# Kernel optimization log

Measured on AMD Instinct MI355X. Metric: run time of the kernel, lower is better.

Reference implementation:

```python
import jax, jax.numpy as jnp
import numpy as np

EMBED = 1024
HEADS = 16
HEAD_DIM = EMBED // HEADS
EPS = 1e-8


def setup_inputs() -> dict:
    key = jax.random.key(0)
    ks = jax.random.split(key, 10)
    s = 1.0 / np.sqrt(EMBED)
    return {
        "hidden_input": jax.random.normal(ks[0], (4, 2048, EMBED), dtype=jnp.float32),
        "Wq": jax.random.uniform(ks[1], (EMBED, EMBED), jnp.float32, -s, s),
        "bq": jax.random.uniform(ks[2], (EMBED,), jnp.float32, -s, s),
        "Wk": jax.random.uniform(ks[3], (EMBED, EMBED), jnp.float32, -s, s),
        "bk": jax.random.uniform(ks[4], (EMBED,), jnp.float32, -s, s),
        "Wv": jax.random.uniform(ks[5], (EMBED, EMBED), jnp.float32, -s, s),
        "bv": jax.random.uniform(ks[6], (EMBED,), jnp.float32, -s, s),
        "Wp": jax.random.uniform(ks[7], (EMBED, EMBED), jnp.float32, -s, s),
        "bp": jax.random.uniform(ks[8], (EMBED,), jnp.float32, -s, s),
        "gamma": jnp.ones((EMBED,), jnp.float32),
        "beta": jnp.zeros((EMBED,), jnp.float32),
    }


def reference(hidden_input, Wq, bq, Wk, bk, Wv, bv, Wp, bp, gamma, beta):
    n, l, e = hidden_input.shape
    h, d = HEADS, HEAD_DIM

    def split_heads(x):  # [n, l, e] -> [n, h, l, d]
        return x.reshape(n, l, h, d).transpose(0, 2, 1, 3)

    q = split_heads(hidden_input @ Wq + bq)
    k = split_heads(hidden_input @ Wk + bk)
    v = split_heads(hidden_input @ Wv + bv)

    scores = jnp.einsum("nhqd,nhkd->nhqk", q, k) / jnp.sqrt(jnp.float32(d))
    attn = jax.nn.softmax(scores, axis=-1)
    ctx = jnp.einsum("nhqk,nhkd->nhqd", attn, v)
    ctx = ctx.transpose(0, 2, 1, 3).reshape(n, l, e)

    out = ctx @ Wp + bp
    x = out + hidden_input
    mu = jnp.mean(x, axis=-1, keepdims=True)
    var = jnp.mean(jnp.square(x - mu), axis=-1, keepdims=True)
    return (x - mu) / jnp.sqrt(var + EPS) * gamma + beta
```

## Files before the change

kernel.cpp:

```cpp
#include <hip/hip_runtime.h>

#define EMBED 1024
#define SEQ   2048
#define BATCH 4
#define HEADS 16

typedef __attribute__((ext_vector_type(8))) short short8;
typedef __attribute__((ext_vector_type(4))) float floatx4;

#define MFMA16(a, b, c) __builtin_amdgcn_mfma_f32_16x16x32_bf16((a), (b), (c), 0, 0, 0)
#define ATT_SCALE (0.125f * 1.44269504088896340736f)

static __device__ __forceinline__ unsigned short f2bf(float f) {
  union { float f; unsigned int u; } v; v.f = f;
  unsigned int u = v.u;
  u += 0x7fffu + ((u >> 16) & 1u);
  return (unsigned short)(u >> 16);
}

static __device__ __forceinline__ void async16(const unsigned short* g, unsigned short* l) {
  __builtin_amdgcn_global_load_lds(
      (const __attribute__((address_space(1))) void*)g,
      (__attribute__((address_space(3))) void*)l, 16, 0, 0);
}

__global__ __launch_bounds__(256) void k_cvt(const float* __restrict__ src,
                                             unsigned short* __restrict__ dst, int n8) {
  int i = blockIdx.x * 256 + threadIdx.x;
  if (i >= n8) return;
  const float4* s = (const float4*)src;
  float4 a = s[i * 2], b = s[i * 2 + 1];
  uint4 o;
  o.x = (unsigned)f2bf(a.x) | ((unsigned)f2bf(a.y) << 16);
  o.y = (unsigned)f2bf(a.z) | ((unsigned)f2bf(a.w) << 16);
  o.z = (unsigned)f2bf(b.x) | ((unsigned)f2bf(b.y) << 16);
  o.w = (unsigned)f2bf(b.z) | ((unsigned)f2bf(b.w) << 16);
  ((uint4*)dst)[i] = o;
}

__global__ __launch_bounds__(256) void k_wt(const float* __restrict__ Wq, const float* __restrict__ Wk,
                                            const float* __restrict__ Wv, const float* __restrict__ Wp,
                                            unsigned short* __restrict__ WT) {
  int z = blockIdx.z;
  const float* src = (z == 0) ? Wq : (z == 1) ? Wk : (z == 2) ? Wv : Wp;
  unsigned short* dst = WT + (size_t)z * EMBED * EMBED;
  int k0 = blockIdx.x * 64, n0 = blockIdx.y * 64;
  __shared__ unsigned short tile[64][65];
  int tid = threadIdx.x;
  for (int i = tid; i < 4096; i += 256) {
    int r = i >> 6, c = i & 63;
    tile[c][r] = f2bf(src[(size_t)(k0 + r) * EMBED + n0 + c]);
  }
  __syncthreads();
  for (int i = tid; i < 4096; i += 256) {
    int r = i >> 6, c = i & 63;
    dst[(size_t)(n0 + r) * EMBED + k0 + c] = tile[r][c];
  }
}

__global__ __launch_bounds__(256) void k_gemm_qkv(const unsigned short* __restrict__ A,
                                                  const unsigned short* __restrict__ BT,
                                                  const float* __restrict__ bq,
                                                  const float* __restrict__ bk,
                                                  const float* __restrict__ bv,
                                                  unsigned short* __restrict__ C) {
  __shared__ unsigned short Als[128 * 32];
  __shared__ unsigned short Bls[128 * 32];
  const int tid = threadIdx.x;
  const int m0 = blockIdx.y * 128, n0 = blockIdx.x * 128;
  const int w = tid >> 6, lane = tid & 63, l16 = lane & 15, quad = lane >> 4;
  const int wrow = (w >> 1) * 64, wcol = (w & 1) * 64;

  floatx4 acc[4][4];
#pragma unroll
  for (int i = 0; i < 4; ++i)
#pragma unroll
    for (int j = 0; j < 4; ++j) acc[i][j] = {0.f, 0.f, 0.f, 0.f};

  const int srow = tid >> 2;
  const int scol = (((tid & 3) ^ ((tid >> 3) & 3)) * 8);
  const unsigned short* Ap = A + (size_t)(m0 + srow) * EMBED + scol;
  const unsigned short* Bp = BT + (size_t)(n0 + srow) * EMBED + scol;

  for (int kt = 0; kt < 32; ++kt) {
    const int k0 = kt * 32;
    async16(Ap + k0, Als + tid * 8);
    async16(Ap + 64 * EMBED + k0, Als + 2048 + tid * 8);
    async16(Bp + k0, Bls + tid * 8);
    async16(Bp + 64 * EMBED + k0, Bls + 2048 + tid * 8);
    __syncthreads();
    short8 af[4], bf[4];
#pragma unroll
    for (int mt = 0; mt < 4; ++mt) {
      int row = wrow + mt * 16 + l16;
      af[mt] = *(const short8*)(Als + row * 32 + ((quad ^ ((row >> 1) & 3)) * 8));
    }
#pragma unroll
    for (int nt = 0; nt < 4; ++nt) {
      int row = wcol + nt * 16 + l16;
      bf[nt] = *(const short8*)(Bls + row * 32 + ((quad ^ ((row >> 1) & 3)) * 8));
    }
#pragma unroll
    for (int mt = 0; mt < 4; ++mt)
#pragma unroll
      for (int nt = 0; nt < 4; ++nt)
        acc[mt][nt] = MFMA16(af[mt], bf[nt], acc[mt][nt]);
    __syncthreads();
  }

  const float* bsel = (n0 < 1024) ? bq : (n0 < 2048 ? bk : bv);
  const int nb = n0 & 1023;
  float bias[4];
#pragma unroll
  for (int nt = 0; nt < 4; ++nt) bias[nt] = bsel[nb + wcol + nt * 16 + l16];
#pragma unroll
  for (int mt = 0; mt < 4; ++mt)
#pragma unroll
    for (int r = 0; r < 4; ++r) {
      int gm = m0 + wrow + mt * 16 + quad * 4 + r;
      size_t base = (size_t)gm * 3072 + n0 + wcol;
#pragma unroll
      for (int nt = 0; nt < 4; ++nt)
        C[base + nt * 16 + l16] = f2bf(acc[mt][nt][r] + bias[nt]);
    }
}

__global__ __launch_bounds__(256) void k_vt(const unsigned short* __restrict__ QKV,
                                            unsigned short* __restrict__ VT) {
  int lt = blockIdx.x;
  int bh = blockIdx.y;
  int b = bh >> 4, h = bh & 15;
  int l0 = lt * 64;
  __shared__ unsigned short tile[64][65];
  const unsigned short* src = QKV + (size_t)(b * SEQ) * 3072 + 2048 + h * 64;
  unsigned short* dst = VT + (size_t)bh * 64 * SEQ;
  int tid = threadIdx.x;
  for (int i = tid; i < 4096; i += 256) {
    int r = i >> 6, c = i & 63;
    tile[c][r] = src[(size_t)(l0 + r) * 3072 + c];
  }
  __syncthreads();
  for (int i = tid; i < 4096; i += 256) {
    int r = i >> 6, c = i & 63;
    dst[(size_t)r * SEQ + l0 + c] = tile[r][c];
  }
}

__global__ __launch_bounds__(256, 2) void k_attn(const unsigned short* __restrict__ QKV,
                                                 const unsigned short* __restrict__ VT,
                                                 unsigned short* __restrict__ CTX) {
  const int qt = blockIdx.x, bh = blockIdx.y;
  const int b = bh >> 4, h = bh & 15;
  const int tid = threadIdx.x;
  const int w = tid >> 6, lane = tid & 63, l16 = lane & 15, quad = lane >> 4;

  __shared__ unsigned short Kls[64 * 64];
  __shared__ unsigned short Vls[64 * 64];
  __shared__ unsigned short Pls[4][64 * 64];

  const unsigned short* Qb = QKV + (size_t)(b * SEQ + qt * 256 + w * 64) * 3072 + h * 64;
  const unsigned short* Kb = QKV + (size_t)(b * SEQ) * 3072 + 1024 + h * 64;
  const unsigned short* Vb = VT + (size_t)bh * 64 * SEQ;
  unsigned short* Pw = Pls[w];

  short8 qf[4][2];
#pragma unroll
  for (int mt = 0; mt < 4; ++mt)
#pragma unroll
    for (int kc = 0; kc < 2; ++kc)
      qf[mt][kc] = *(const short8*)(Qb + (size_t)(mt * 16 + l16) * 3072 + kc * 32 + quad * 8);

  floatx4 o[4][4];
  float rs[4][4];
#pragma unroll
  for (int mt = 0; mt < 4; ++mt)
#pragma unroll
    for (int nt = 0; nt < 4; ++nt) { o[mt][nt] = {0.f, 0.f, 0.f, 0.f}; rs[mt][nt] = 0.f; }

  const int srow = tid >> 3;
  const int scol = (((tid & 7) ^ (srow & 7)) * 8);

  for (int kt = 0; kt < 32; ++kt) {
    const int kv0 = kt * 64;
    async16(Kb + (size_t)(kv0 + srow) * 3072 + scol, Kls + tid * 8);
    async16(Kb + (size_t)(kv0 + 32 + srow) * 3072 + scol, Kls + 2048 + tid * 8);
    async16(Vb + (size_t)srow * SEQ + kv0 + scol, Vls + tid * 8);
    async16(Vb + (size_t)(32 + srow) * SEQ + kv0 + scol, Vls + 2048 + tid * 8);
    __syncthreads();

    short8 kf[4][2];
#pragma unroll
    for (int nt = 0; nt < 4; ++nt)
#pragma unroll
      for (int kc = 0; kc < 2; ++kc) {
        int row = nt * 16 + l16;
        kf[nt][kc] = *(const short8*)(Kls + row * 64 + (((kc * 4 + quad) ^ (row & 7)) * 8));
      }

#pragma unroll
    for (int mt = 0; mt < 4; ++mt) {
      floatx4 s[4];
#pragma unroll
      for (int nt = 0; nt < 4; ++nt) {
        floatx4 z = {0.f, 0.f, 0.f, 0.f};
        z = MFMA16(qf[mt][0], kf[nt][0], z);
        s[nt] = MFMA16(qf[mt][1], kf[nt][1], z);
      }
#pragma unroll
      for (int nt = 0; nt < 4; ++nt)
#pragma unroll
        for (int r = 0; r < 4; ++r) {
          float p = exp2f(s[nt][r] * ATT_SCALE);
          rs[mt][r] += p;
          int row = mt * 16 + quad * 4 + r;
          int col = nt * 16 + l16;
          union { float f; unsigned u; } cv; cv.f = p;
          Pw[row * 64 + (((col >> 3) ^ (row & 7)) * 8) + (col & 7)] = (unsigned short)(cv.u >> 16);
        }
    }

    __asm__ volatile("s_waitcnt lgkmcnt(0)" ::: "memory");

    short8 vf[4][2];
#pragma unroll
    for (int nt = 0; nt < 4; ++nt)
#pragma unroll
      for (int kc = 0; kc < 2; ++kc) {
        int row = nt * 16 + l16;
        vf[nt][kc] = *(const short8*)(Vls + row * 64 + (((kc * 4 + quad) ^ (row & 7)) * 8));
      }
#pragma unroll
    for (int kc = 0; kc < 2; ++kc)
#pragma unroll
      for (int mt = 0; mt < 4; ++mt) {
        int row = mt * 16 + l16;
        short8 pf = *(const short8*)(Pw + row * 64 + (((kc * 4 + quad) ^ (row & 7)) * 8));
#pragma unroll
        for (int nt = 0; nt < 4; ++nt)
          o[mt][nt] = MFMA16(pf, vf[nt][kc], o[mt][nt]);
      }
    __syncthreads();
  }

#pragma unroll
  for (int mt = 0; mt < 4; ++mt)
#pragma unroll
    for (int r = 0; r < 4; ++r) {
      float v = rs[mt][r];
#pragma unroll
      for (int off = 1; off < 16; off <<= 1) v += __shfl_xor(v, off);
      rs[mt][r] = 1.f / v;
    }

#pragma unroll
  for (int mt = 0; mt < 4; ++mt)
#pragma unroll
    for (int r = 0; r < 4; ++r) {
      int gq = b * SEQ + qt * 256 + w * 64 + mt * 16 + quad * 4 + r;
      float inv = rs[mt][r];
      size_t base = (size_t)gq * EMBED + h * 64;
#pragma unroll
      for (int nt = 0; nt < 4; ++nt)
        CTX[base + nt * 16 + l16] = f2bf(o[mt][nt][r] * inv);
    }
}

__global__ __launch_bounds__(256) void k_gemm_proj(const unsigned short* __restrict__ A,
                                                   const unsigned short* __restrict__ BT,
                                                   const float* __restrict__ bp,
                                                   const float* __restrict__ hid,
                                                   float* __restrict__ X) {
  __shared__ unsigned short Als[128 * 32];
  __shared__ unsigned short Bls[128 * 32];
  const int tid = threadIdx.x;
  const int m0 = blockIdx.y * 128, n0 = blockIdx.x * 128;
  const int w = tid >> 6, lane = tid & 63, l16 = lane & 15, quad = lane >> 4;
  const int wrow = (w >> 1) * 64, wcol = (w & 1) * 64;

  floatx4 acc[4][4];
#pragma unroll
  for (int i = 0; i < 4; ++i)
#pragma unroll
    for (int j = 0; j < 4; ++j) acc[i][j] = {0.f, 0.f, 0.f, 0.f};

  const int srow = tid >> 2;
  const int scol = (((tid & 3) ^ ((tid >> 3) & 3)) * 8);
  const unsigned short* Ap = A + (size_t)(m0 + srow) * EMBED + scol;
  const unsigned short* Bp = BT + (size_t)(n0 + srow) * EMBED + scol;

  for (int kt = 0; kt < 32; ++kt) {
    const int k0 = kt * 32;
    async16(Ap + k0, Als + tid * 8);
    async16(Ap + 64 * EMBED + k0, Als + 2048 + tid * 8);
    async16(Bp + k0, Bls + tid * 8);
    async16(Bp + 64 * EMBED + k0, Bls + 2048 + tid * 8);
    __syncthreads();
    short8 af[4], bf[4];
#pragma unroll
    for (int mt = 0; mt < 4; ++mt) {
      int row = wrow + mt * 16 + l16;
      af[mt] = *(const short8*)(Als + row * 32 + ((quad ^ ((row >> 1) & 3)) * 8));
    }
#pragma unroll
    for (int nt = 0; nt < 4; ++nt) {
      int row = wcol + nt * 16 + l16;
      bf[nt] = *(const short8*)(Bls + row * 32 + ((quad ^ ((row >> 1) & 3)) * 8));
    }
#pragma unroll
    for (int mt = 0; mt < 4; ++mt)
#pragma unroll
      for (int nt = 0; nt < 4; ++nt)
        acc[mt][nt] = MFMA16(af[mt], bf[nt], acc[mt][nt]);
    __syncthreads();
  }

  float bias[4];
#pragma unroll
  for (int nt = 0; nt < 4; ++nt) bias[nt] = bp[n0 + wcol + nt * 16 + l16];
#pragma unroll
  for (int mt = 0; mt < 4; ++mt)
#pragma unroll
    for (int r = 0; r < 4; ++r) {
      int gm = m0 + wrow + mt * 16 + quad * 4 + r;
      size_t base = (size_t)gm * EMBED + n0 + wcol;
#pragma unroll
      for (int nt = 0; nt < 4; ++nt) {
        size_t idx = base + nt * 16 + l16;
        X[idx] = acc[mt][nt][r] + bias[nt] + hid[idx];
      }
    }
}

__global__ __launch_bounds__(256) void k_ln(float* __restrict__ x,
                                            const float* __restrict__ gamma,
                                            const float* __restrict__ beta) {
  int row = blockIdx.x, tid = threadIdx.x;
  float4* rp = (float4*)(x + (size_t)row * EMBED);
  float4 v = rp[tid];
  float s = v.x + v.y + v.z + v.w;
  float q = v.x * v.x + v.y * v.y + v.z * v.z + v.w * v.w;
#pragma unroll
  for (int off = 1; off < 64; off <<= 1) {
    s += __shfl_xor(s, off);
    q += __shfl_xor(q, off);
  }
  __shared__ float ss[4], sq[4];
  int w = tid >> 6;
  if ((tid & 63) == 0) { ss[w] = s; sq[w] = q; }
  __syncthreads();
  s = ss[0] + ss[1] + ss[2] + ss[3];
  q = sq[0] + sq[1] + sq[2] + sq[3];
  float mean = s * (1.f / 1024.f);
  float var = q * (1.f / 1024.f) - mean * mean;
  float rstd = rsqrtf(var + 1e-8f);
  float4 g = ((const float4*)gamma)[tid];
  float4 be = ((const float4*)beta)[tid];
  v.x = (v.x - mean) * rstd * g.x + be.x;
  v.y = (v.y - mean) * rstd * g.y + be.y;
  v.z = (v.z - mean) * rstd * g.z + be.z;
  v.w = (v.w - mean) * rstd * g.w + be.w;
  rp[tid] = v;
}

extern "C" void kernel_launch(void* const* d_in, const int* in_sizes, int n_in,
                              void* d_out, int out_size, void* d_ws, size_t ws_size,
                              hipStream_t stream) {
  const float* hid   = (const float*)d_in[0];
  const float* Wq    = (const float*)d_in[1];
  const float* bq    = (const float*)d_in[2];
  const float* Wk    = (const float*)d_in[3];
  const float* bk    = (const float*)d_in[4];
  const float* Wv    = (const float*)d_in[5];
  const float* bv    = (const float*)d_in[6];
  const float* Wp    = (const float*)d_in[7];
  const float* bp    = (const float*)d_in[8];
  const float* gamma = (const float*)d_in[9];
  const float* beta  = (const float*)d_in[10];
  float* out = (float*)d_out;

  char* ws = (char*)d_ws;
  unsigned short* hidA = (unsigned short*)ws;
  unsigned short* WT   = (unsigned short*)(ws + (size_t)(16 << 20));
  unsigned short* QKV  = (unsigned short*)(ws + (size_t)(24 << 20));
  unsigned short* VT   = (unsigned short*)(ws + (size_t)(72 << 20));
  unsigned short* CTX  = (unsigned short*)(ws + (size_t)(88 << 20));

  k_cvt<<<4096, 256, 0, stream>>>(hid, hidA, (BATCH * SEQ * EMBED) / 8);
  k_wt<<<dim3(16, 16, 4), 256, 0, stream>>>(Wq, Wk, Wv, Wp, WT);
  k_gemm_qkv<<<dim3(24, 64), 256, 0, stream>>>(hidA, WT, bq, bk, bv, QKV);
  k_vt<<<dim3(32, 64), 256, 0, stream>>>(QKV, VT);
  k_attn<<<dim3(8, 64), 256, 0, stream>>>(QKV, VT, CTX);
  k_gemm_proj<<<dim3(8, 64), 256, 0, stream>>>(CTX, WT + (size_t)3 * EMBED * EMBED, bp, hid, out);
  k_ln<<<8192, 256, 0, stream>>>(out, gamma, beta);
}
```

Baseline: 340.7 us.

## Double-buffer K/V tiles in attention and split P into half-tiles

The attention kernel now double-buffers the K and V shared-memory tiles, prefetching tile kt+1 while tile kt is computed, which removes one barrier per iteration. The 64-column P tile is processed in two 32-column halves with a smaller padded and rotated P buffer. The smaller P buffer is meant to free LDS so that three blocks fit per CU. The grid axes are swapped so consecutive blocks cover different heads for the same query tile. The exchange is more complex indexing and higher register pressure under the tighter launch bound, and the single remaining barrier must still protect P reuse and buffer swaps correctly.

```diff
diff --git a/kernel.cpp b/kernel.cpp
--- a/kernel.cpp
+++ b/kernel.cpp
@@ -146,23 +146,32 @@
   }
 }
 
-__global__ __launch_bounds__(256, 2) void k_attn(const unsigned short* __restrict__ QKV,
+__global__ __launch_bounds__(256, 3) void k_attn(const unsigned short* __restrict__ QKV,
                                                  const unsigned short* __restrict__ VT,
                                                  unsigned short* __restrict__ CTX) {
-  const int qt = blockIdx.x, bh = blockIdx.y;
+  const int bh = blockIdx.x, qt = blockIdx.y;
   const int b = bh >> 4, h = bh & 15;
   const int tid = threadIdx.x;
   const int w = tid >> 6, lane = tid & 63, l16 = lane & 15, quad = lane >> 4;
-
-  __shared__ unsigned short Kls[64 * 64];
-  __shared__ unsigned short Vls[64 * 64];
-  __shared__ unsigned short Pls[4][64 * 64];
+  const int l7 = l16 & 7, h8 = l16 >> 3;
+
+  __shared__ unsigned short Kls[2][4096];
+  __shared__ unsigned short Vls[2][4096];
+  __shared__ unsigned short Pls[4][2560];
 
   const unsigned short* Qb = QKV + (size_t)(b * SEQ + qt * 256 + w * 64) * 3072 + h * 64;
   const unsigned short* Kb = QKV + (size_t)(b * SEQ) * 3072 + 1024 + h * 64;
   const unsigned short* Vb = VT + (size_t)bh * 64 * SEQ;
   unsigned short* Pw = Pls[w];
 
+  int pwb[4];
+#pragma unroll
+  for (int c0 = 0; c0 < 4; ++c0)
+    pwb[c0] = quad * 160 + (((h8 + quad + c0) & 3) << 3) + l7;
+  const int prb = l16 * 40 + (((quad + l16 + (l16 >> 2)) & 3) << 3);
+  const int sl0 = l16 * 64 + ((quad ^ l7) << 3);
+  const int sl1 = l16 * 64 + (((4 ^ quad) ^ l7) << 3);
+
   short8 qf[4][2];
 #pragma unroll
   for (int mt = 0; mt < 4; ++mt)
@@ -180,66 +189,65 @@
   const int srow = tid >> 3;
   const int scol = (((tid & 7) ^ (srow & 7)) * 8);
 
+  async16(Kb + (size_t)srow * 3072 + scol, Kls[0] + tid * 8);
+  async16(Kb + (size_t)(32 + srow) * 3072 + scol, Kls[0] + 2048 + tid * 8);
+  async16(Vb + (size_t)srow * SEQ + scol, Vls[0] + tid * 8);
+  async16(Vb + (size_t)(32 + srow) * SEQ + scol, Vls[0] + 2048 + tid * 8);
+
   for (int kt = 0; kt < 32; ++kt) {
-    const int kv0 = kt * 64;
-    async16(Kb + (size_t)(kv0 + srow) * 3072 + scol, Kls + tid * 8);
-    async16(Kb + (size_t)(kv0 + 32 + srow) * 3072 + scol, Kls + 2048 + tid * 8);
-    async16(Vb + (size_t)srow * SEQ + kv0 + scol, Vls + tid * 8);
-    async16(Vb + (size_t)(32 + srow) * SEQ + kv0 + scol, Vls + 2048 + tid * 8);
+    const int cur = kt & 1;
     __syncthreads();
-
-    short8 kf[4][2];
-#pragma unroll
-    for (int nt = 0; nt < 4; ++nt)
-#pragma unroll
-      for (int kc = 0; kc < 2; ++kc) {
-        int row = nt * 16 + l16;
-        kf[nt][kc] = *(const short8*)(Kls + row * 64 + (((kc * 4 + quad) ^ (row & 7)) * 8));
+    if (kt < 31) {
+      const int kv1 = (kt + 1) * 64;
+      async16(Kb + (size_t)(kv1 + srow) * 3072 + scol, Kls[cur ^ 1] + tid * 8);
+      async16(Kb + (size_t)(kv1 + 32 + srow) * 3072 + scol, Kls[cur ^ 1] + 2048 + tid * 8);
+      async16(Vb + (size_t)srow * SEQ + kv1 + scol, Vls[cur ^ 1] + tid * 8);
+      async16(Vb + (size_t)(32 + srow) * SEQ + kv1 + scol, Vls[cur ^ 1] + 2048 + tid * 8);
+    }
+    const unsigned short* K0 = Kls[cur];
+    const unsigned short* V0 = Vls[cur];
+
+#pragma unroll
+    for (int p = 0; p < 2; ++p) {
+      short8 kf[2][2];
+#pragma unroll
+      for (int ntp = 0; ntp < 2; ++ntp) {
+        kf[ntp][0] = *(const short8*)(K0 + sl0 + (2 * p + ntp) * 1024);
+        kf[ntp][1] = *(const short8*)(K0 + sl1 + (2 * p + ntp) * 1024);
       }
-
-#pragma unroll
-    for (int mt = 0; mt < 4; ++mt) {
-      floatx4 s[4];
-#pragma unroll
-      for (int nt = 0; nt < 4; ++nt) {
-        floatx4 z = {0.f, 0.f, 0.f, 0.f};
-        z = MFMA16(qf[mt][0], kf[nt][0], z);
-        s[nt] = MFMA16(qf[mt][1], kf[nt][1], z);
+#pragma unroll
+      for (int mt = 0; mt < 4; ++mt) {
+        floatx4 s0 = {0.f, 0.f, 0.f, 0.f}, s1 = {0.f, 0.f, 0.f, 0.f};
+        s0 = MFMA16(qf[mt][0], kf[0][0], s0);
+        s0 = MFMA16(qf[mt][1], kf[0][1], s0);
+        s1 = MFMA16(qf[mt][0], kf[1][0], s1);
+        s1 = MFMA16(qf[mt][1], kf[1][1], s1);
+#pragma unroll
+        for (int r = 0; r < 4; ++r) {
+          float p0 = exp2f(s0[r] * ATT_SCALE);
+          float p1 = exp2f(s1[r] * ATT_SCALE);
+          rs[mt][r] += p0 + p1;
+          union { float f; unsigned u; } c0v, c1v;
+          c0v.f = p0; c1v.f = p1;
+          Pw[pwb[r & 3] + (mt * 16 + r) * 40] = (unsigned short)(c0v.u >> 16);
+          Pw[pwb[(2 + r) & 3] + (mt * 16 + r) * 40] = (unsigned short)(c1v.u >> 16);
+        }
       }
+      __asm__ volatile("s_waitcnt lgkmcnt(0)" ::: "memory");
+
+      short8 vf[4];
 #pragma unroll
       for (int nt = 0; nt < 4; ++nt)
-#pragma unroll
-        for (int r = 0; r < 4; ++r) {
-          float p = exp2f(s[nt][r] * ATT_SCALE);
-          rs[mt][r] += p;
-          int row = mt * 16 + quad * 4 + r;
-          int col = nt * 16 + l16;
-          union { float f; unsigned u; } cv; cv.f = p;
-          Pw[row * 64 + (((col >> 3) ^ (row & 7)) * 8) + (col & 7)] = (unsigned short)(cv.u >> 16);
-        }
-    }
-
-    __asm__ volatile("s_waitcnt lgkmcnt(0)" ::: "memory");
-
-    short8 vf[4][2];
-#pragma unroll
-    for (int nt = 0; nt < 4; ++nt)
-#pragma unroll
-      for (int kc = 0; kc < 2; ++kc) {
-        int row = nt * 16 + l16;
-        vf[nt][kc] = *(const short8*)(Vls + row * 64 + (((kc * 4 + quad) ^ (row & 7)) * 8));
+        vf[nt] = *(const short8*)(V0 + (p ? sl1 : sl0) + nt * 1024);
+#pragma unroll
+      for (int mt = 0; mt < 4; ++mt) {
+        short8 pf = *(const short8*)(Pw + prb + mt * 640);
+#pragma unroll
+        for (int nt = 0; nt < 4; ++nt)
+          o[mt][nt] = MFMA16(pf, vf[nt], o[mt][nt]);
       }
-#pragma unroll
-    for (int kc = 0; kc < 2; ++kc)
-#pragma unroll
-      for (int mt = 0; mt < 4; ++mt) {
-        int row = mt * 16 + l16;
-        short8 pf = *(const short8*)(Pw + row * 64 + (((kc * 4 + quad) ^ (row & 7)) * 8));
-#pragma unroll
-        for (int nt = 0; nt < 4; ++nt)
-          o[mt][nt] = MFMA16(pf, vf[nt][kc], o[mt][nt]);
-      }
-    __syncthreads();
+      __asm__ volatile("" ::: "memory");
+    }
   }
 
 #pragma unroll
@@ -389,7 +397,7 @@
   k_wt<<<dim3(16, 16, 4), 256, 0, stream>>>(Wq, Wk, Wv, Wp, WT);
   k_gemm_qkv<<<dim3(24, 64), 256, 0, stream>>>(hidA, WT, bq, bk, bv, QKV);
   k_vt<<<dim3(32, 64), 256, 0, stream>>>(QKV, VT);
-  k_attn<<<dim3(8, 64), 256, 0, stream>>>(QKV, VT, CTX);
+  k_attn<<<dim3(64, 8), 256, 0, stream>>>(QKV, VT, CTX);
   k_gemm_proj<<<dim3(8, 64), 256, 0, stream>>>(CTX, WT + (size_t)3 * EMBED * EMBED, bp, hid, out);
   k_ln<<<8192, 256, 0, stream>>>(out, gamma, beta);
 }
```

After: 398.7 us. 1.17x slower.

## Double-buffer attention K/V loads, widen GEMM K-tile, and swap grid order

Applied to the files above, without the earlier changes.

The attention kernel now double-buffers K and V in shared memory. It prefetches the next tile right after the barrier, which removes the trailing barrier each iteration and overlaps global loads with compute. The P-tile write/read addressing switches to a rotated layout with precomputed offsets. Both GEMMs move from a K-tile of 32 to 64 with an 8-wide XOR swizzle, halving barrier count, and all three main kernels swap grid dimensions so consecutive blocks share the weight/K column tile. The cost is more LDS per block, which may lower occupancy, plus higher register pressure from loading V fragments early.

```diff
diff --git a/kernel.cpp b/kernel.cpp
--- a/kernel.cpp
+++ b/kernel.cpp
@@ -64,11 +64,12 @@
                                                   const float* __restrict__ bk,
                                                   const float* __restrict__ bv,
                                                   unsigned short* __restrict__ C) {
-  __shared__ unsigned short Als[128 * 32];
-  __shared__ unsigned short Bls[128 * 32];
+  __shared__ unsigned short Als[128 * 64];
+  __shared__ unsigned short Bls[128 * 64];
   const int tid = threadIdx.x;
-  const int m0 = blockIdx.y * 128, n0 = blockIdx.x * 128;
+  const int m0 = blockIdx.x * 128, n0 = blockIdx.y * 128;
   const int w = tid >> 6, lane = tid & 63, l16 = lane & 15, quad = lane >> 4;
+  const int l7 = l16 & 7;
   const int wrow = (w >> 1) * 64, wcol = (w & 1) * 64;
 
   floatx4 acc[4][4];
@@ -77,34 +78,45 @@
 #pragma unroll
     for (int j = 0; j < 4; ++j) acc[i][j] = {0.f, 0.f, 0.f, 0.f};
 
-  const int srow = tid >> 2;
-  const int scol = (((tid & 3) ^ ((tid >> 3) & 3)) * 8);
+  const int srow = tid >> 3;
+  const int scol = (((tid & 7) ^ (srow & 7)) * 8);
   const unsigned short* Ap = A + (size_t)(m0 + srow) * EMBED + scol;
   const unsigned short* Bp = BT + (size_t)(n0 + srow) * EMBED + scol;
 
-  for (int kt = 0; kt < 32; ++kt) {
-    const int k0 = kt * 32;
-    async16(Ap + k0, Als + tid * 8);
-    async16(Ap + 64 * EMBED + k0, Als + 2048 + tid * 8);
-    async16(Bp + k0, Bls + tid * 8);
-    async16(Bp + 64 * EMBED + k0, Bls + 2048 + tid * 8);
+  int ab[2], bb[2];
+#pragma unroll
+  for (int kc = 0; kc < 2; ++kc) {
+    ab[kc] = (wrow + l16) * 64 + (((4 * kc + quad) ^ l7) << 3);
+    bb[kc] = (wcol + l16) * 64 + (((4 * kc + quad) ^ l7) << 3);
+  }
+
+  for (int kt = 0; kt < 16; ++kt) {
+    const int k0 = kt * 64;
+#pragma unroll
+    for (int i = 0; i < 4; ++i)
+      async16(Ap + k0 + (size_t)i * 32 * EMBED, Als + i * 2048 + tid * 8);
+#pragma unroll
+    for (int i = 0; i < 4; ++i)
+      async16(Bp + k0 + (size_t)i * 32 * EMBED, Bls + i * 2048 + tid * 8);
     __syncthreads();
-    short8 af[4], bf[4];
-#pragma unroll
-    for (int mt = 0; mt < 4; ++mt) {
-      int row = wrow + mt * 16 + l16;
-      af[mt] = *(const short8*)(Als + row * 32 + ((quad ^ ((row >> 1) & 3)) * 8));
-    }
-#pragma unroll
-    for (int nt = 0; nt < 4; ++nt) {
-      int row = wcol + nt * 16 + l16;
-      bf[nt] = *(const short8*)(Bls + row * 32 + ((quad ^ ((row >> 1) & 3)) * 8));
-    }
+    short8 af[4][2], bf[4][2];
 #pragma unroll
     for (int mt = 0; mt < 4; ++mt)
 #pragma unroll
-      for (int nt = 0; nt < 4; ++nt)
-        acc[mt][nt] = MFMA16(af[mt], bf[nt], acc[mt][nt]);
+      for (int kc = 0; kc < 2; ++kc)
+        af[mt][kc] = *(const short8*)(Als + ab[kc] + mt * 1024);
+#pragma unroll
+    for (int nt = 0; nt < 4; ++nt)
+#pragma unroll
+      for (int kc = 0; kc < 2; ++kc)
+        bf[nt][kc] = *(const short8*)(Bls + bb[kc] + nt * 1024);
+#pragma unroll
+    for (int kc = 0; kc < 2; ++kc)
+#pragma unroll
+      for (int mt = 0; mt < 4; ++mt)
+#pragma unroll
+        for (int nt = 0; nt < 4; ++nt)
+          acc[mt][nt] = MFMA16(af[mt][kc], bf[nt][kc], acc[mt][nt]);
     __syncthreads();
   }
 
@@ -149,20 +161,32 @@
 __global__ __launch_bounds__(256, 2) void k_attn(const unsigned short* __restrict__ QKV,
                                                  const unsigned short* __restrict__ VT,
                                                  unsigned short* __restrict__ CTX) {
-  const int qt = blockIdx.x, bh = blockIdx.y;
+  const int bh = blockIdx.x, qt = blockIdx.y;
   const int b = bh >> 4, h = bh & 15;
   const int tid = threadIdx.x;
   const int w = tid >> 6, lane = tid & 63, l16 = lane & 15, quad = lane >> 4;
-
-  __shared__ unsigned short Kls[64 * 64];
-  __shared__ unsigned short Vls[64 * 64];
-  __shared__ unsigned short Pls[4][64 * 64];
+  const int l7 = l16 & 7, h8 = l16 >> 3;
+
+  __shared__ unsigned short Kls[2][4096];
+  __shared__ unsigned short Vls[2][4096];
+  __shared__ unsigned short Pls[4][4096];
 
   const unsigned short* Qb = QKV + (size_t)(b * SEQ + qt * 256 + w * 64) * 3072 + h * 64;
   const unsigned short* Kb = QKV + (size_t)(b * SEQ) * 3072 + 1024 + h * 64;
   const unsigned short* Vb = VT + (size_t)bh * 64 * SEQ;
   unsigned short* Pw = Pls[w];
 
+  int pwb[8];
+#pragma unroll
+  for (int s = 0; s < 8; ++s)
+    pwb[s] = quad * 256 + (((h8 + 4 * quad + s) & 7) << 3) + l7;
+  int prb[2], kvb[2];
+#pragma unroll
+  for (int kc = 0; kc < 2; ++kc) {
+    prb[kc] = l16 * 64 + (((4 * kc + quad + l16) & 7) << 3);
+    kvb[kc] = l16 * 64 + (((4 * kc + quad) ^ l7) << 3);
+  }
+
   short8 qf[4][2];
 #pragma unroll
   for (int mt = 0; mt < 4; ++mt)
@@ -180,21 +204,31 @@
   const int srow = tid >> 3;
   const int scol = (((tid & 7) ^ (srow & 7)) * 8);
 
+  async16(Kb + (size_t)srow * 3072 + scol, Kls[0] + tid * 8);
+  async16(Kb + (size_t)(32 + srow) * 3072 + scol, Kls[0] + 2048 + tid * 8);
+  async16(Vb + (size_t)srow * SEQ + scol, Vls[0] + tid * 8);
+  async16(Vb + (size_t)(32 + srow) * SEQ + scol, Vls[0] + 2048 + tid * 8);
+
   for (int kt = 0; kt < 32; ++kt) {
-    const int kv0 = kt * 64;
-    async16(Kb + (size_t)(kv0 + srow) * 3072 + scol, Kls + tid * 8);
-    async16(Kb + (size_t)(kv0 + 32 + srow) * 3072 + scol, Kls + 2048 + tid * 8);
-    async16(Vb + (size_t)srow * SEQ + kv0 + scol, Vls + tid * 8);
-    async16(Vb + (size_t)(32 + srow) * SEQ + kv0 + scol, Vls + 2048 + tid * 8);
+    const int cur = kt & 1;
     __syncthreads();
-
-    short8 kf[4][2];
+    if (kt < 31) {
+      const int kv1 = (kt + 1) * 64;
+      async16(Kb + (size_t)(kv1 + srow) * 3072 + scol, Kls[cur ^ 1] + tid * 8);
+      async16(Kb + (size_t)(kv1 + 32 + srow) * 3072 + scol, Kls[cur ^ 1] + 2048 + tid * 8);
+      async16(Vb + (size_t)srow * SEQ + kv1 + scol, Vls[cur ^ 1] + tid * 8);
+      async16(Vb + (size_t)(32 + srow) * SEQ + kv1 + scol, Vls[cur ^ 1] + 2048 + tid * 8);
+    }
+    const unsigned short* K0 = Kls[cur];
+    const unsigned short* V0 = Vls[cur];
+
+    short8 kf[4][2], vf[4][2];
 #pragma unroll
     for (int nt = 0; nt < 4; ++nt)
 #pragma unroll
       for (int kc = 0; kc < 2; ++kc) {
-        int row = nt * 16 + l16;
-        kf[nt][kc] = *(const short8*)(Kls + row * 64 + (((kc * 4 + quad) ^ (row & 7)) * 8));
+        kf[nt][kc] = *(const short8*)(K0 + kvb[kc] + nt * 1024);
+        vf[nt][kc] = *(const short8*)(V0 + kvb[kc] + nt * 1024);
       }
 
 #pragma unroll
@@ -212,34 +246,21 @@
         for (int r = 0; r < 4; ++r) {
           float p = exp2f(s[nt][r] * ATT_SCALE);
           rs[mt][r] += p;
-          int row = mt * 16 + quad * 4 + r;
-          int col = nt * 16 + l16;
           union { float f; unsigned u; } cv; cv.f = p;
-          Pw[row * 64 + (((col >> 3) ^ (row & 7)) * 8) + (col & 7)] = (unsigned short)(cv.u >> 16);
+          Pw[pwb[(r + 2 * nt) & 7] + mt * 1024 + r * 64] = (unsigned short)(cv.u >> 16);
         }
     }
-
     __asm__ volatile("s_waitcnt lgkmcnt(0)" ::: "memory");
 
-    short8 vf[4][2];
-#pragma unroll
-    for (int nt = 0; nt < 4; ++nt)
-#pragma unroll
-      for (int kc = 0; kc < 2; ++kc) {
-        int row = nt * 16 + l16;
-        vf[nt][kc] = *(const short8*)(Vls + row * 64 + (((kc * 4 + quad) ^ (row & 7)) * 8));
-      }
 #pragma unroll
     for (int kc = 0; kc < 2; ++kc)
 #pragma unroll
       for (int mt = 0; mt < 4; ++mt) {
-        int row = mt * 16 + l16;
-        short8 pf = *(const short8*)(Pw + row * 64 + (((kc * 4 + quad) ^ (row & 7)) * 8));
+        short8 pf = *(const short8*)(Pw + prb[kc] + mt * 1024);
 #pragma unroll
         for (int nt = 0; nt < 4; ++nt)
           o[mt][nt] = MFMA16(pf, vf[nt][kc], o[mt][nt]);
       }
-    __syncthreads();
   }
 
 #pragma unroll
@@ -270,11 +291,12 @@
                                                    const float* __restrict__ bp,
                                                    const float* __restrict__ hid,
                                                    float* __restrict__ X) {
-  __shared__ unsigned short Als[128 * 32];
-  __shared__ unsigned short Bls[128 * 32];
+  __shared__ unsigned short Als[128 * 64];
+  __shared__ unsigned short Bls[128 * 64];
   const int tid = threadIdx.x;
-  const int m0 = blockIdx.y * 128, n0 = blockIdx.x * 128;
+  const int m0 = blockIdx.x * 128, n0 = blockIdx.y * 128;
   const int w = tid >> 6, lane = tid & 63, l16 = lane & 15, quad = lane >> 4;
+  const int l7 = l16 & 7;
   const int wrow = (w >> 1) * 64, wcol = (w & 1) * 64;
 
   floatx4 acc[4][4];
@@ -283,34 +305,45 @@
 #pragma unroll
     for (int j = 0; j < 4; ++j) acc[i][j] = {0.f, 0.f, 0.f, 0.f};
 
-  const int srow = tid >> 2;
-  const int scol = (((tid & 3) ^ ((tid >> 3) & 3)) * 8);
+  const int srow = tid >> 3;
+  const int scol = (((tid & 7) ^ (srow & 7)) * 8);
   const unsigned short* Ap = A + (size_t)(m0 + srow) * EMBED + scol;
   const unsigned short* Bp = BT + (size_t)(n0 + srow) * EMBED + scol;
 
-  for (int kt = 0; kt < 32; ++kt) {
-    const int k0 = kt * 32;
-    async16(Ap + k0, Als + tid * 8);
-    async16(Ap + 64 * EMBED + k0, Als + 2048 + tid * 8);
-    async16(Bp + k0, Bls + tid * 8);
-    async16(Bp + 64 * EMBED + k0, Bls + 2048 + tid * 8);
+  int ab[2], bb[2];
+#pragma unroll
+  for (int kc = 0; kc < 2; ++kc) {
+    ab[kc] = (wrow + l16) * 64 + (((4 * kc + quad) ^ l7) << 3);
+    bb[kc] = (wcol + l16) * 64 + (((4 * kc + quad) ^ l7) << 3);
+  }
+
+  for (int kt = 0; kt < 16; ++kt) {
+    const int k0 = kt * 64;
+#pragma unroll
+    for (int i = 0; i < 4; ++i)
+      async16(Ap + k0 + (size_t)i * 32 * EMBED, Als + i * 2048 + tid * 8);
+#pragma unroll
+    for (int i = 0; i < 4; ++i)
+      async16(Bp + k0 + (size_t)i * 32 * EMBED, Bls + i * 2048 + tid * 8);
     __syncthreads();
-    short8 af[4], bf[4];
-#pragma unroll
-    for (int mt = 0; mt < 4; ++mt) {
-      int row = wrow + mt * 16 + l16;
-      af[mt] = *(const short8*)(Als + row * 32 + ((quad ^ ((row >> 1) & 3)) * 8));
-    }
-#pragma unroll
-    for (int nt = 0; nt < 4; ++nt) {
-      int row = wcol + nt * 16 + l16;
-      bf[nt] = *(const short8*)(Bls + row * 32 + ((quad ^ ((row >> 1) & 3)) * 8));
-    }
+    short8 af[4][2], bf[4][2];
 #pragma unroll
     for (int mt = 0; mt < 4; ++mt)
 #pragma unroll
-      for (int nt = 0; nt < 4; ++nt)
-        acc[mt][nt] = MFMA16(af[mt], bf[nt], acc[mt][nt]);
+      for (int kc = 0; kc < 2; ++kc)
+        af[mt][kc] = *(const short8*)(Als + ab[kc] + mt * 1024);
+#pragma unroll
+    for (int nt = 0; nt < 4; ++nt)
+#pragma unroll
+      for (int kc = 0; kc < 2; ++kc)
+        bf[nt][kc] = *(const short8*)(Bls + bb[kc] + nt * 1024);
+#pragma unroll
+    for (int kc = 0; kc < 2; ++kc)
+#pragma unroll
+      for (int mt = 0; mt < 4; ++mt)
+#pragma unroll
+        for (int nt = 0; nt < 4; ++nt)
+          acc[mt][nt] = MFMA16(af[mt][kc], bf[nt][kc], acc[mt][nt]);
     __syncthreads();
   }
 
@@ -387,9 +420,9 @@
 
   k_cvt<<<4096, 256, 0, stream>>>(hid, hidA, (BATCH * SEQ * EMBED) / 8);
   k_wt<<<dim3(16, 16, 4), 256, 0, stream>>>(Wq, Wk, Wv, Wp, WT);
-  k_gemm_qkv<<<dim3(24, 64), 256, 0, stream>>>(hidA, WT, bq, bk, bv, QKV);
+  k_gemm_qkv<<<dim3(64, 24), 256, 0, stream>>>(hidA, WT, bq, bk, bv, QKV);
   k_vt<<<dim3(32, 64), 256, 0, stream>>>(QKV, VT);
-  k_attn<<<dim3(8, 64), 256, 0, stream>>>(QKV, VT, CTX);
-  k_gemm_proj<<<dim3(8, 64), 256, 0, stream>>>(CTX, WT + (size_t)3 * EMBED * EMBED, bp, hid, out);
+  k_attn<<<dim3(64, 8), 256, 0, stream>>>(QKV, VT, CTX);
+  k_gemm_proj<<<dim3(64, 8), 256, 0, stream>>>(CTX, WT + (size_t)3 * EMBED * EMBED, bp, hid, out);
   k_ln<<<8192, 256, 0, stream>>>(out, gamma, beta);
 }
```

New measurement: 365.5 us. 7.3% more time.
